# Kernel tuning notes

Measured on AMD Instinct MI355X. Metric: run time of the kernel, lower is better.

Reference implementation:

```python
import jax, jax.numpy as jnp
import numpy as np

N, E, F_IN, HID, HEADS, CLASSES = 50000, 800000, 128, 128, 4, 2
NEG_SLOPE = 0.2


def _gatv2_layer(x, Wl, Wr, att, bias, src, dst, heads, concat):
    # PyG GATv2Conv (share_weights=False, eval mode):
    #   e_ij = att . leaky_relu(Wl x_j + Wr x_i); alpha = segment_softmax over dst;
    #   out_i = sum_j alpha_ij * (Wl x_j)
    n = x.shape[0]
    c = att.shape[-1]
    xl = (x @ Wl).reshape(n, heads, c)   # source transform [N,H,C]
    xr = (x @ Wr).reshape(n, heads, c)   # target transform [N,H,C]
    e = jax.nn.leaky_relu(xl[src] + xr[dst], NEG_SLOPE)      # [E,H,C]
    logits = jnp.einsum('ehc,hc->eh', e, att)                # [E,H]
    m = jax.ops.segment_max(logits, dst, num_segments=n)     # stable softmax per dst
    p = jnp.exp(logits - m[dst])
    denom = jax.ops.segment_sum(p, dst, num_segments=n)
    alpha = p / (denom[dst] + 1e-16)                         # [E,H]
    out = jax.ops.segment_sum(alpha[:, :, None] * xl[src], dst, num_segments=n)  # [N,H,C]
    out = out.reshape(n, heads * c) if concat else out.mean(axis=1)
    return out + bias


def setup_inputs() -> dict:
    key = jax.random.key(0)
    ks = jax.random.split(key, 16)
    s = lambda fan_in: 1.0 / np.sqrt(fan_in)
    inp = {
        'x': jax.random.normal(ks[0], (N, F_IN), jnp.float32),
        'edge_idx': jax.random.randint(ks[1], (2, E), 0, N, jnp.int64),
        'w_in': jax.random.normal(ks[2], (F_IN, HID), jnp.float32) * s(F_IN),
        'b_in': jnp.zeros((HID,), jnp.float32),
        'wl1': jax.random.normal(ks[3], (HID, HEADS * HID), jnp.float32) * s(HID),
        'wr1': jax.random.normal(ks[4], (HID, HEADS * HID), jnp.float32) * s(HID),
        'att1': jax.random.normal(ks[5], (HEADS, HID), jnp.float32) * s(HID),
        'b1': jnp.zeros((HEADS * HID,), jnp.float32),
        'wl2': jax.random.normal(ks[6], (HEADS * HID, HID), jnp.float32) * s(HEADS * HID),
        'wr2': jax.random.normal(ks[7], (HEADS * HID, HID), jnp.float32) * s(HEADS * HID),
        'att2': jax.random.normal(ks[8], (1, HID), jnp.float32) * s(HID),
        'b2': jnp.zeros((HID,), jnp.float32),
        'w_out': jax.random.normal(ks[9], (HID, CLASSES), jnp.float32) * s(HID),
        'b_out': jnp.zeros((CLASSES,), jnp.float32),
    }
    return inp


def reference(x, edge_idx, w_in, b_in, wl1, wr1, att1, b1, wl2, wr2, att2, b2, w_out, b_out):
    n = x.shape[0]
    loops = jnp.arange(n, dtype=edge_idx.dtype)  # PyG add_self_loops=True
    src = jnp.concatenate([edge_idx[0], loops])
    dst = jnp.concatenate([edge_idx[1], loops])
    h = jax.nn.elu(x @ w_in + b_in)              # dropout is identity in eval
    h = jax.nn.elu(_gatv2_layer(h, wl1, wr1, att1, b1, src, dst, HEADS, True))
    h = jax.nn.elu(_gatv2_layer(h, wl2, wr2, att2, b2, src, dst, 1, False))
    logits = h @ w_out + b_out
    return jax.nn.log_softmax(logits, axis=1)
```

## Files before the change

kernel.cpp:

```cpp
#include <hip/hip_runtime.h>
#include <hip/hip_bf16.h>
#include <math.h>

#define F_IN   128
#define HID    128
#define HEADS  4
#define HC1    (HEADS*HID)
#define CLASSES 2
#define NEG_SLOPE 0.2f

#define SCAN_CHUNK 2048

typedef __attribute__((ext_vector_type(8))) short short8;
typedef __attribute__((ext_vector_type(4))) float f32x4;

__global__ void zero_int_kernel(int* __restrict__ p, int n) {
    int i = blockIdx.x * blockDim.x + threadIdx.x;
    int stride = gridDim.x * blockDim.x;
    for (; i < n; i += stride) p[i] = 0;
}

__global__ void deg_kernel(const int* __restrict__ dst_arr, int* __restrict__ deg,
                           int E, int N) {
    int e = blockIdx.x * blockDim.x + threadIdx.x;
    if (e >= E) return;
    int d = dst_arr[e];
    if ((unsigned)d >= (unsigned)N) d = 0;
    atomicAdd(&deg[d], 1);
}

__global__ void scan_partial_kernel(const int* __restrict__ deg, int* __restrict__ bsum, int n) {
    __shared__ int sdata[256];
    int b = blockIdx.x, t = threadIdx.x;
    int base = b * SCAN_CHUNK;
    int s = 0;
    for (int i = t; i < SCAN_CHUNK; i += 256) {
        int idx = base + i;
        s += (idx < n) ? deg[idx] : 0;
    }
    sdata[t] = s;
    __syncthreads();
    for (int off = 128; off; off >>= 1) {
        if (t < off) sdata[t] += sdata[t + off];
        __syncthreads();
    }
    if (t == 0) bsum[b] = sdata[0];
}

__global__ void scan_bsums_kernel(int* __restrict__ bsum, int nb, int* __restrict__ row, int n) {
    if (blockIdx.x == 0 && threadIdx.x == 0) {
        int acc = 0;
        for (int i = 0; i < nb; ++i) { int v = bsum[i]; bsum[i] = acc; acc += v; }
        row[n] = acc;
    }
}

__global__ void scan_final_kernel(const int* __restrict__ deg, const int* __restrict__ bsum,
                                  int* __restrict__ row, int* __restrict__ cursor, int n) {
    __shared__ int tsum[256];
    int b = blockIdx.x, t = threadIdx.x;
    int base = b * SCAN_CHUNK + t * 8;
    int local[8];
    int s = 0;
    #pragma unroll
    for (int k = 0; k < 8; ++k) {
        int idx = base + k;
        int v = (idx < n) ? deg[idx] : 0;
        local[k] = s;
        s += v;
    }
    tsum[t] = s;
    __syncthreads();
    for (int off = 1; off < 256; off <<= 1) {
        int v = 0;
        if (t >= off) v = tsum[t - off];
        __syncthreads();
        if (t >= off) tsum[t] += v;
        __syncthreads();
    }
    int texcl = (t == 0) ? 0 : tsum[t - 1];
    int boff = bsum[b];
    #pragma unroll
    for (int k = 0; k < 8; ++k) {
        int idx = base + k;
        if (idx < n) {
            int v = boff + texcl + local[k];
            row[idx] = v;
            cursor[idx] = v;
        }
    }
}

__global__ void scatter_kernel(const int* __restrict__ src_arr, const int* __restrict__ dst_arr,
                               int* __restrict__ cursor, int* __restrict__ src_sorted,
                               int E, int N) {
    int e = blockIdx.x * blockDim.x + threadIdx.x;
    if (e >= E) return;
    int s = src_arr[e], d = dst_arr[e];
    if ((unsigned)s >= (unsigned)N) s = 0;
    if ((unsigned)d >= (unsigned)N) d = 0;
    int pos = atomicAdd(&cursor[d], 1);
    src_sorted[pos] = s;
}

__global__ void transpose_to_bf16_kernel(const float* __restrict__ w,
                                         __hip_bfloat16* __restrict__ wT,
                                         int K, int N) {
    int t = blockIdx.x * blockDim.x + threadIdx.x;
    if (t >= K * N) return;
    int n = t / K, k = t % K;
    wT[t] = __float2bfloat16(w[(size_t)k * N + n]);
}

__global__ void f32_to_bf16_kernel(const float* __restrict__ in,
                                   __hip_bfloat16* __restrict__ outb, int n) {
    int i = blockIdx.x * blockDim.x + threadIdx.x;
    int stride = gridDim.x * blockDim.x;
    short* ob = (short*)outb;
    for (int base = i * 4; base < n; base += stride * 4) {
        float4 v = *(const float4*)(in + base);
        __hip_bfloat16 h0 = __float2bfloat16(v.x);
        __hip_bfloat16 h1 = __float2bfloat16(v.y);
        __hip_bfloat16 h2 = __float2bfloat16(v.z);
        __hip_bfloat16 h3 = __float2bfloat16(v.w);
        short4 sv;
        sv.x = *reinterpret_cast<short*>(&h0);
        sv.y = *reinterpret_cast<short*>(&h1);
        sv.z = *reinterpret_cast<short*>(&h2);
        sv.w = *reinterpret_cast<short*>(&h3);
        *(short4*)(ob + base) = sv;
    }
}

template<int ACT, typename OutT>
__global__ __launch_bounds__(256) void mfma_gemm_kernel(
    const __hip_bfloat16* __restrict__ A,
    const __hip_bfloat16* __restrict__ BT,
    const float* __restrict__ bias,
    OutT* __restrict__ C,
    int M, int K, int N)
{
    constexpr int BM = 128, BN = 64, BK = 64, LDA = 72;
    __shared__ __align__(16) short As[BM * LDA];
    __shared__ __align__(16) short Bs[BN * LDA];

    const int tid  = threadIdx.x;
    const int lane = tid & 63;
    const int wid  = tid >> 6;
    const int wm   = wid >> 1;
    const int wn   = wid & 1;
    const int fr   = lane & 15;
    const int fk   = (lane >> 4) * 8;

    const int row0 = blockIdx.y * BM;
    const int col0 = blockIdx.x * BN;

    const short* Ag = (const short*)A;
    const short* Bg = (const short*)BT;

    f32x4 acc[4][2] = {};

    for (int k0 = 0; k0 < K; k0 += BK) {
        #pragma unroll
        for (int it = 0; it < 4; ++it) {
            int chunk = it * 256 + tid;
            int r = chunk >> 3, c = chunk & 7;
            int gr = row0 + r;
            short8 v = {0, 0, 0, 0, 0, 0, 0, 0};
            if (gr < M) v = *(const short8*)(Ag + (size_t)gr * K + k0 + c * 8);
            *(short8*)(&As[r * LDA + c * 8]) = v;
        }
        #pragma unroll
        for (int it = 0; it < 2; ++it) {
            int chunk = it * 256 + tid;
            int n = chunk >> 3, c = chunk & 7;
            short8 v = *(const short8*)(Bg + (size_t)(col0 + n) * K + k0 + c * 8);
            *(short8*)(&Bs[n * LDA + c * 8]) = v;
        }
        __syncthreads();
        #pragma unroll
        for (int kk = 0; kk < 2; ++kk) {
            short8 af[4], bf[2];
            #pragma unroll
            for (int i = 0; i < 4; ++i)
                af[i] = *(const short8*)(&As[(wm * 64 + i * 16 + fr) * LDA + kk * 32 + fk]);
            #pragma unroll
            for (int j = 0; j < 2; ++j)
                bf[j] = *(const short8*)(&Bs[(wn * 32 + j * 16 + fr) * LDA + kk * 32 + fk]);
            #pragma unroll
            for (int i = 0; i < 4; ++i)
                #pragma unroll
                for (int j = 0; j < 2; ++j)
                    acc[i][j] = __builtin_amdgcn_mfma_f32_16x16x32_bf16(af[i], bf[j], acc[i][j], 0, 0, 0);
        }
        __syncthreads();
    }

    const int crow = row0 + wm * 64;
    const int ccol = col0 + wn * 32;
    #pragma unroll
    for (int i = 0; i < 4; ++i) {
        #pragma unroll
        for (int j = 0; j < 2; ++j) {
            int col = ccol + j * 16 + (lane & 15);
            float bv = bias ? bias[col] : 0.0f;
            #pragma unroll
            for (int reg = 0; reg < 4; ++reg) {
                int r = crow + i * 16 + (lane >> 4) * 4 + reg;
                if (r < M) {
                    float v = acc[i][j][reg] + bv;
                    if (ACT == 1) v = (v > 0.0f) ? v : expm1f(v);
                    C[(size_t)r * N + col] = (OutT)v;
                }
            }
        }
    }
}

__global__ __launch_bounds__(256) void gatv2_l1_fused_kernel(
    const __hip_bfloat16* __restrict__ xlr,
    const int* __restrict__ row, const int* __restrict__ src_sorted,
    const float* __restrict__ att, const float* __restrict__ b1,
    __hip_bfloat16* __restrict__ out1, int N)
{
    int d = blockIdx.x * 4 + (threadIdx.x >> 6);
    if (d >= N) return;
    int lane = threadIdx.x & 63;
    int cbase = lane * 8;
    const short* base = (const short*)xlr;

    float xrd[8], attv[8];
    {
        uint4 raw = *reinterpret_cast<const uint4*>(base + (size_t)d * 1024 + 512 + cbase);
        const unsigned* u = reinterpret_cast<const unsigned*>(&raw);
        #pragma unroll
        for (int j = 0; j < 4; ++j) {
            xrd[2 * j]     = __uint_as_float(u[j] << 16);
            xrd[2 * j + 1] = __uint_as_float(u[j] & 0xffff0000u);
        }
        #pragma unroll
        for (int k = 0; k < 8; ++k) attv[k] = att[cbase + k];
    }

    float m = -__builtin_huge_valf();
    float s = 0.0f;
    float o[8] = {};

    int rs = row[d], re = row[d + 1];

    uint4 raw = *reinterpret_cast<const uint4*>(base + (size_t)d * 1024 + cbase);
    for (int it = rs - 1; it < re; ++it) {
        uint4 cur = raw;
        if (it + 1 < re) {
            int sn = src_sorted[it + 1];
            raw = *reinterpret_cast<const uint4*>(base + (size_t)sn * 1024 + cbase);
        }
        float v[8];
        const unsigned* u = reinterpret_cast<const unsigned*>(&cur);
        #pragma unroll
        for (int j = 0; j < 4; ++j) {
            v[2 * j]     = __uint_as_float(u[j] << 16);
            v[2 * j + 1] = __uint_as_float(u[j] & 0xffff0000u);
        }
        float t = 0.0f;
        #pragma unroll
        for (int k = 0; k < 8; ++k) {
            float e = v[k] + xrd[k];
            e = (e > 0.0f) ? e : NEG_SLOPE * e;
            t = fmaf(e, attv[k], t);
        }
        t += __shfl_xor(t, 1);
        t += __shfl_xor(t, 2);
        t += __shfl_xor(t, 4);
        t += __shfl_xor(t, 8);
        if (t > m) {
            float r = __expf(m - t);
            s *= r;
            #pragma unroll
            for (int k = 0; k < 8; ++k) o[k] *= r;
            m = t;
        }
        float p = __expf(t - m);
        s += p;
        #pragma unroll
        for (int k = 0; k < 8; ++k) o[k] = fmaf(p, v[k], o[k]);
    }

    float inv = 1.0f / (s + 1e-16f);
    short8 sv;
    #pragma unroll
    for (int k = 0; k < 8; ++k) {
        float val = o[k] * inv + b1[cbase + k];
        val = (val > 0.0f) ? val : expm1f(val);
        __hip_bfloat16 hb = __float2bfloat16(val);
        sv[k] = *reinterpret_cast<short*>(&hb);
    }
    *(short8*)((short*)out1 + (size_t)d * HC1 + cbase) = sv;
}

__global__ __launch_bounds__(256) void gatv2_l2_final_kernel(
    const __hip_bfloat16* __restrict__ xlr2,
    const int* __restrict__ row, const int* __restrict__ src_sorted,
    const float* __restrict__ att2, const float* __restrict__ b2,
    const float* __restrict__ w_out, const float* __restrict__ b_out,
    float* __restrict__ out, int N)
{
    int d = blockIdx.x * 4 + (threadIdx.x >> 6);
    if (d >= N) return;
    int lane = threadIdx.x & 63;
    int c0 = lane * 2;
    const short* base = (const short*)xlr2;

    unsigned xr_raw = *reinterpret_cast<const unsigned*>(base + (size_t)d * 256 + 128 + c0);
    float xrd0 = __uint_as_float(xr_raw << 16);
    float xrd1 = __uint_as_float(xr_raw & 0xffff0000u);
    float2 attv = *reinterpret_cast<const float2*>(att2 + c0);

    float m = -__builtin_huge_valf();
    float s = 0.0f;
    float o0 = 0.0f, o1 = 0.0f;

    int rs = row[d], re = row[d + 1];
    unsigned raw = *reinterpret_cast<const unsigned*>(base + (size_t)d * 256 + c0);
    for (int it = rs - 1; it < re; ++it) {
        unsigned cur = raw;
        if (it + 1 < re) {
            int sn = src_sorted[it + 1];
            raw = *reinterpret_cast<const unsigned*>(base + (size_t)sn * 256 + c0);
        }
        float v0 = __uint_as_float(cur << 16);
        float v1 = __uint_as_float(cur & 0xffff0000u);
        float e0 = v0 + xrd0; e0 = (e0 > 0.0f) ? e0 : NEG_SLOPE * e0;
        float e1 = v1 + xrd1; e1 = (e1 > 0.0f) ? e1 : NEG_SLOPE * e1;
        float t = fmaf(e0, attv.x, e1 * attv.y);
        #pragma unroll
        for (int off = 32; off; off >>= 1) t += __shfl_xor(t, off);
        if (t > m) {
            float r = __expf(m - t);
            s *= r; o0 *= r; o1 *= r;
            m = t;
        }
        float p = __expf(t - m);
        s += p;
        o0 = fmaf(p, v0, o0);
        o1 = fmaf(p, v1, o1);
    }

    float inv = 1.0f / (s + 1e-16f);
    float h0v = o0 * inv + b2[c0];
    float h1v = o1 * inv + b2[c0 + 1];
    h0v = (h0v > 0.0f) ? h0v : expm1f(h0v);
    h1v = (h1v > 0.0f) ? h1v : expm1f(h1v);

    float a0 = fmaf(h0v, w_out[c0 * 2 + 0], h1v * w_out[(c0 + 1) * 2 + 0]);
    float a1 = fmaf(h0v, w_out[c0 * 2 + 1], h1v * w_out[(c0 + 1) * 2 + 1]);
    #pragma unroll
    for (int off = 32; off; off >>= 1) {
        a0 += __shfl_xor(a0, off);
        a1 += __shfl_xor(a1, off);
    }
    if (lane == 0) {
        float z0 = a0 + b_out[0];
        float z1 = a1 + b_out[1];
        float mx = fmaxf(z0, z1);
        float lse = mx + logf(__expf(z0 - mx) + __expf(z1 - mx));
        out[(size_t)d * CLASSES + 0] = z0 - lse;
        out[(size_t)d * CLASSES + 1] = z1 - lse;
    }
}

extern "C" void kernel_launch(void* const* d_in, const int* in_sizes, int n_in,
                              void* d_out, int out_size, void* d_ws, size_t ws_size,
                              hipStream_t stream)
{
    const float* x     = (const float*)d_in[0];
    const int*   eidx  = (const int*)d_in[1];
    const float* w_in  = (const float*)d_in[2];
    const float* b_in  = (const float*)d_in[3];
    const float* wl1   = (const float*)d_in[4];
    const float* wr1   = (const float*)d_in[5];
    const float* att1  = (const float*)d_in[6];
    const float* b1    = (const float*)d_in[7];
    const float* wl2   = (const float*)d_in[8];
    const float* wr2   = (const float*)d_in[9];
    const float* att2  = (const float*)d_in[10];
    const float* b2    = (const float*)d_in[11];
    const float* w_out = (const float*)d_in[12];
    const float* b_out = (const float*)d_in[13];
    float* out = (float*)d_out;

    const int N = in_sizes[0] / F_IN;
    const int E = in_sizes[1] / 2;
    const int* src_arr = eidx;
    const int* dst_arr = eidx + E;

    size_t off = 0;
    auto alloc = [&](size_t bytes) -> char* {
        char* ptr = (char*)d_ws + off;
        off += (bytes + 255) & ~(size_t)255;
        return ptr;
    };
    int* row        = (int*)alloc((size_t)(N + 1) * 4);
    int* cursor     = (int*)alloc((size_t)N * 4);
    int* deg        = (int*)alloc((size_t)N * 4);
    int* bsum       = (int*)alloc(64 * 4);
    int* src_sorted = (int*)alloc((size_t)E * 4);
    __hip_bfloat16* w_inT = (__hip_bfloat16*)alloc((size_t)F_IN * HID * 2);
    __hip_bfloat16* wT1   = (__hip_bfloat16*)alloc((size_t)2 * HC1 * HID * 2);
    __hip_bfloat16* wT2   = (__hip_bfloat16*)alloc((size_t)2 * HID * HC1 * 2);
    __hip_bfloat16* xb    = (__hip_bfloat16*)alloc((size_t)N * F_IN * 2);
    __hip_bfloat16* h0b   = (__hip_bfloat16*)alloc((size_t)N * HID * 2);
    __hip_bfloat16* xlr1  = (__hip_bfloat16*)alloc((size_t)N * 2 * HC1 * 2);
    __hip_bfloat16* out1  = (__hip_bfloat16*)alloc((size_t)N * HC1 * 2);

    __hip_bfloat16* xlr2 = xlr1;

    dim3 blk(256);
    const int NB_SCAN = (N + SCAN_CHUNK - 1) / SCAN_CHUNK;

    hipLaunchKernelGGL(zero_int_kernel, dim3(64), blk, 0, stream, deg, N);
    hipLaunchKernelGGL(deg_kernel, dim3((E + 255) / 256), blk, 0, stream, dst_arr, deg, E, N);
    hipLaunchKernelGGL(scan_partial_kernel, dim3(NB_SCAN), blk, 0, stream, deg, bsum, N);
    hipLaunchKernelGGL(scan_bsums_kernel, dim3(1), blk, 0, stream, bsum, NB_SCAN, row, N);
    hipLaunchKernelGGL(scan_final_kernel, dim3(NB_SCAN), blk, 0, stream, deg, bsum, row, cursor, N);
    hipLaunchKernelGGL(scatter_kernel, dim3((E + 255) / 256), blk, 0, stream,
                       src_arr, dst_arr, cursor, src_sorted, E, N);

    {
        dim3 gw((HID * HC1 + 255) / 256);
        dim3 gwi((F_IN * HID + 255) / 256);
        hipLaunchKernelGGL(transpose_to_bf16_kernel, gwi, blk, 0, stream, w_in, w_inT, F_IN, HID);
        hipLaunchKernelGGL(transpose_to_bf16_kernel, gw, blk, 0, stream, wl1, wT1, HID, HC1);
        hipLaunchKernelGGL(transpose_to_bf16_kernel, gw, blk, 0, stream, wr1, wT1 + (size_t)HC1 * HID, HID, HC1);
        hipLaunchKernelGGL(transpose_to_bf16_kernel, gw, blk, 0, stream, wl2, wT2, HC1, HID);
        hipLaunchKernelGGL(transpose_to_bf16_kernel, gw, blk, 0, stream, wr2, wT2 + (size_t)HID * HC1, HC1, HID);
    }

    hipLaunchKernelGGL(f32_to_bf16_kernel, dim3(2048), blk, 0, stream, x, xb, N * F_IN);
    {
        dim3 grid(HID / 64, (N + 127) / 128);
        hipLaunchKernelGGL((mfma_gemm_kernel<1, __hip_bfloat16>), grid, blk, 0, stream,
                           xb, w_inT, b_in, h0b, N, F_IN, HID);
    }
    {
        dim3 grid(2 * HC1 / 64, (N + 127) / 128);
        hipLaunchKernelGGL((mfma_gemm_kernel<0, __hip_bfloat16>), grid, blk, 0, stream,
                           h0b, wT1, (const float*)nullptr, xlr1, N, HID, 2 * HC1);
    }
    {
        dim3 grid((N + 3) / 4);
        hipLaunchKernelGGL(gatv2_l1_fused_kernel, grid, blk, 0, stream,
                           xlr1, row, src_sorted, att1, b1, out1, N);
    }
    {
        dim3 grid(2 * HID / 64, (N + 127) / 128);
        hipLaunchKernelGGL((mfma_gemm_kernel<0, __hip_bfloat16>), grid, blk, 0, stream,
                           out1, wT2, (const float*)nullptr, xlr2, N, HC1, 2 * HID);
    }
    {
        dim3 grid((N + 3) / 4);
        hipLaunchKernelGGL(gatv2_l2_final_kernel, grid, blk, 0, stream,
                           xlr2, row, src_sorted, att2, b2, w_out, b_out, out, N);
    }
}
```

Before: 603.2 us.

## Split xl/xr buffers, widen GEMM tile, merge weight prep, use exp2 softmax

Splits the interleaved xl/xr projection buffer into separate contiguous arrays so the gather kernels read rows with a smaller stride (HC1 or HID instead of 1024 or 256). Source rows then pack more densely for cache reuse. The GEMM tile grows from 128x64 to 128x128, reusing each A tile across more columns at the cost of more accumulator registers. The five weight-transpose launches merge into one kernel, and layer-2 outputs reuse the xb and h0b buffers. The softmax folds log2(e) into the attention vector so it can use exp2f, and leaky_relu becomes fmaxf.

```diff
diff --git a/kernel.cpp b/kernel.cpp
--- a/kernel.cpp
+++ b/kernel.cpp
@@ -8,6 +8,7 @@
 #define HC1    (HEADS*HID)
 #define CLASSES 2
 #define NEG_SLOPE 0.2f
+#define LOG2E 1.44269504088896340736f
 
 #define SCAN_CHUNK 2048
 
@@ -103,13 +104,25 @@
     src_sorted[pos] = s;
 }
 
-__global__ void transpose_to_bf16_kernel(const float* __restrict__ w,
-                                         __hip_bfloat16* __restrict__ wT,
-                                         int K, int N) {
+__global__ void weights_prep_kernel(
+    const float* __restrict__ w_in, const float* __restrict__ wl1,
+    const float* __restrict__ wr1, const float* __restrict__ wl2,
+    const float* __restrict__ wr2,
+    __hip_bfloat16* __restrict__ w_inT, __hip_bfloat16* __restrict__ wT1l,
+    __hip_bfloat16* __restrict__ wT1r, __hip_bfloat16* __restrict__ wT2l,
+    __hip_bfloat16* __restrict__ wT2r)
+{
     int t = blockIdx.x * blockDim.x + threadIdx.x;
-    if (t >= K * N) return;
-    int n = t / K, k = t % K;
-    wT[t] = __float2bfloat16(w[(size_t)k * N + n]);
+    const int S0 = 128 * 128, S1 = 128 * 512;
+    const float* w; __hip_bfloat16* wT; int K, Nn, idx;
+    if (t < S0)                { w = w_in; wT = w_inT; K = 128; Nn = 128; idx = t; }
+    else if (t < S0 + S1)      { w = wl1;  wT = wT1l;  K = 128; Nn = 512; idx = t - S0; }
+    else if (t < S0 + 2 * S1)  { w = wr1;  wT = wT1r;  K = 128; Nn = 512; idx = t - S0 - S1; }
+    else if (t < S0 + 3 * S1)  { w = wl2;  wT = wT2l;  K = 512; Nn = 128; idx = t - S0 - 2 * S1; }
+    else if (t < S0 + 4 * S1)  { w = wr2;  wT = wT2r;  K = 512; Nn = 128; idx = t - S0 - 3 * S1; }
+    else return;
+    int n = idx / K, k = idx % K;
+    wT[idx] = __float2bfloat16(w[(size_t)k * Nn + n]);
 }
 
 __global__ void f32_to_bf16_kernel(const float* __restrict__ in,
@@ -140,7 +153,7 @@
     OutT* __restrict__ C,
     int M, int K, int N)
 {
-    constexpr int BM = 128, BN = 64, BK = 64, LDA = 72;
+    constexpr int BM = 128, BN = 128, BK = 64, LDA = 72;
     __shared__ __align__(16) short As[BM * LDA];
     __shared__ __align__(16) short Bs[BN * LDA];
 
@@ -158,7 +171,7 @@
     const short* Ag = (const short*)A;
     const short* Bg = (const short*)BT;
 
-    f32x4 acc[4][2] = {};
+    f32x4 acc[4][4] = {};
 
     for (int k0 = 0; k0 < K; k0 += BK) {
         #pragma unroll
@@ -171,7 +184,7 @@
             *(short8*)(&As[r * LDA + c * 8]) = v;
         }
         #pragma unroll
-        for (int it = 0; it < 2; ++it) {
+        for (int it = 0; it < 4; ++it) {
             int chunk = it * 256 + tid;
             int n = chunk >> 3, c = chunk & 7;
             short8 v = *(const short8*)(Bg + (size_t)(col0 + n) * K + k0 + c * 8);
@@ -180,28 +193,28 @@
         __syncthreads();
         #pragma unroll
         for (int kk = 0; kk < 2; ++kk) {
-            short8 af[4], bf[2];
+            short8 af[4], bf[4];
             #pragma unroll
             for (int i = 0; i < 4; ++i)
                 af[i] = *(const short8*)(&As[(wm * 64 + i * 16 + fr) * LDA + kk * 32 + fk]);
             #pragma unroll
-            for (int j = 0; j < 2; ++j)
-                bf[j] = *(const short8*)(&Bs[(wn * 32 + j * 16 + fr) * LDA + kk * 32 + fk]);
+            for (int j = 0; j < 4; ++j)
+                bf[j] = *(const short8*)(&Bs[(wn * 64 + j * 16 + fr) * LDA + kk * 32 + fk]);
             #pragma unroll
             for (int i = 0; i < 4; ++i)
                 #pragma unroll
-                for (int j = 0; j < 2; ++j)
+                for (int j = 0; j < 4; ++j)
                     acc[i][j] = __builtin_amdgcn_mfma_f32_16x16x32_bf16(af[i], bf[j], acc[i][j], 0, 0, 0);
         }
         __syncthreads();
     }
 
     const int crow = row0 + wm * 64;
-    const int ccol = col0 + wn * 32;
+    const int ccol = col0 + wn * 64;
     #pragma unroll
     for (int i = 0; i < 4; ++i) {
         #pragma unroll
-        for (int j = 0; j < 2; ++j) {
+        for (int j = 0; j < 4; ++j) {
             int col = ccol + j * 16 + (lane & 15);
             float bv = bias ? bias[col] : 0.0f;
             #pragma unroll
@@ -218,7 +231,7 @@
 }
 
 __global__ __launch_bounds__(256) void gatv2_l1_fused_kernel(
-    const __hip_bfloat16* __restrict__ xlr,
+    const __hip_bfloat16* __restrict__ xl, const __hip_bfloat16* __restrict__ xr,
     const int* __restrict__ row, const int* __restrict__ src_sorted,
     const float* __restrict__ att, const float* __restrict__ b1,
     __hip_bfloat16* __restrict__ out1, int N)
@@ -227,11 +240,11 @@
     if (d >= N) return;
     int lane = threadIdx.x & 63;
     int cbase = lane * 8;
-    const short* base = (const short*)xlr;
+    const short* xlb = (const short*)xl;
 
     float xrd[8], attv[8];
     {
-        uint4 raw = *reinterpret_cast<const uint4*>(base + (size_t)d * 1024 + 512 + cbase);
+        uint4 raw = *reinterpret_cast<const uint4*>((const short*)xr + (size_t)d * HC1 + cbase);
         const unsigned* u = reinterpret_cast<const unsigned*>(&raw);
         #pragma unroll
         for (int j = 0; j < 4; ++j) {
@@ -239,7 +252,7 @@
             xrd[2 * j + 1] = __uint_as_float(u[j] & 0xffff0000u);
         }
         #pragma unroll
-        for (int k = 0; k < 8; ++k) attv[k] = att[cbase + k];
+        for (int k = 0; k < 8; ++k) attv[k] = att[cbase + k] * LOG2E;
     }
 
     float m = -__builtin_huge_valf();
@@ -248,12 +261,12 @@
 
     int rs = row[d], re = row[d + 1];
 
-    uint4 raw = *reinterpret_cast<const uint4*>(base + (size_t)d * 1024 + cbase);
+    uint4 raw = *reinterpret_cast<const uint4*>(xlb + (size_t)d * HC1 + cbase);
     for (int it = rs - 1; it < re; ++it) {
         uint4 cur = raw;
         if (it + 1 < re) {
             int sn = src_sorted[it + 1];
-            raw = *reinterpret_cast<const uint4*>(base + (size_t)sn * 1024 + cbase);
+            raw = *reinterpret_cast<const uint4*>(xlb + (size_t)sn * HC1 + cbase);
         }
         float v[8];
         const unsigned* u = reinterpret_cast<const unsigned*>(&cur);
@@ -265,8 +278,8 @@
         float t = 0.0f;
         #pragma unroll
         for (int k = 0; k < 8; ++k) {
-            float e = v[k] + xrd[k];
-            e = (e > 0.0f) ? e : NEG_SLOPE * e;
+            float ek = v[k] + xrd[k];
+            float e = fmaxf(ek, NEG_SLOPE * ek);
             t = fmaf(e, attv[k], t);
         }
         t += __shfl_xor(t, 1);
@@ -274,13 +287,13 @@
         t += __shfl_xor(t, 4);
         t += __shfl_xor(t, 8);
         if (t > m) {
-            float r = __expf(m - t);
+            float r = exp2f(m - t);
             s *= r;
             #pragma unroll
             for (int k = 0; k < 8; ++k) o[k] *= r;
             m = t;
         }
-        float p = __expf(t - m);
+        float p = exp2f(t - m);
         s += p;
         #pragma unroll
         for (int k = 0; k < 8; ++k) o[k] = fmaf(p, v[k], o[k]);
@@ -299,7 +312,7 @@
 }
 
 __global__ __launch_bounds__(256) void gatv2_l2_final_kernel(
-    const __hip_bfloat16* __restrict__ xlr2,
+    const __hip_bfloat16* __restrict__ xl2, const __hip_bfloat16* __restrict__ xr2,
     const int* __restrict__ row, const int* __restrict__ src_sorted,
     const float* __restrict__ att2, const float* __restrict__ b2,
     const float* __restrict__ w_out, const float* __restrict__ b_out,
@@ -309,38 +322,39 @@
     if (d >= N) return;
     int lane = threadIdx.x & 63;
     int c0 = lane * 2;
-    const short* base = (const short*)xlr2;
-
-    unsigned xr_raw = *reinterpret_cast<const unsigned*>(base + (size_t)d * 256 + 128 + c0);
+    const short* xlb = (const short*)xl2;
+
+    unsigned xr_raw = *reinterpret_cast<const unsigned*>((const short*)xr2 + (size_t)d * HID + c0);
     float xrd0 = __uint_as_float(xr_raw << 16);
     float xrd1 = __uint_as_float(xr_raw & 0xffff0000u);
-    float2 attv = *reinterpret_cast<const float2*>(att2 + c0);
+    float a2x = att2[c0] * LOG2E;
+    float a2y = att2[c0 + 1] * LOG2E;
 
     float m = -__builtin_huge_valf();
     float s = 0.0f;
     float o0 = 0.0f, o1 = 0.0f;
 
     int rs = row[d], re = row[d + 1];
-    unsigned raw = *reinterpret_cast<const unsigned*>(base + (size_t)d * 256 + c0);
+    unsigned raw = *reinterpret_cast<const unsigned*>(xlb + (size_t)d * HID + c0);
     for (int it = rs - 1; it < re; ++it) {
         unsigned cur = raw;
         if (it + 1 < re) {
             int sn = src_sorted[it + 1];
-            raw = *reinterpret_cast<const unsigned*>(base + (size_t)sn * 256 + c0);
+            raw = *reinterpret_cast<const unsigned*>(xlb + (size_t)sn * HID + c0);
         }
         float v0 = __uint_as_float(cur << 16);
         float v1 = __uint_as_float(cur & 0xffff0000u);
-        float e0 = v0 + xrd0; e0 = (e0 > 0.0f) ? e0 : NEG_SLOPE * e0;
-        float e1 = v1 + xrd1; e1 = (e1 > 0.0f) ? e1 : NEG_SLOPE * e1;
-        float t = fmaf(e0, attv.x, e1 * attv.y);
+        float e0 = v0 + xrd0; e0 = fmaxf(e0, NEG_SLOPE * e0);
+        float e1 = v1 + xrd1; e1 = fmaxf(e1, NEG_SLOPE * e1);
+        float t = fmaf(e0, a2x, e1 * a2y);
         #pragma unroll
         for (int off = 32; off; off >>= 1) t += __shfl_xor(t, off);
         if (t > m) {
-            float r = __expf(m - t);
+            float r = exp2f(m - t);
             s *= r; o0 *= r; o1 *= r;
             m = t;
         }
-        float p = __expf(t - m);
+        float p = exp2f(t - m);
         s += p;
         o0 = fmaf(p, v0, o0);
         o1 = fmaf(p, v1, o1);
@@ -406,14 +420,18 @@
     int* bsum       = (int*)alloc(64 * 4);
     int* src_sorted = (int*)alloc((size_t)E * 4);
     __hip_bfloat16* w_inT = (__hip_bfloat16*)alloc((size_t)F_IN * HID * 2);
-    __hip_bfloat16* wT1   = (__hip_bfloat16*)alloc((size_t)2 * HC1 * HID * 2);
-    __hip_bfloat16* wT2   = (__hip_bfloat16*)alloc((size_t)2 * HID * HC1 * 2);
+    __hip_bfloat16* wT1l  = (__hip_bfloat16*)alloc((size_t)HID * HC1 * 2);
+    __hip_bfloat16* wT1r  = (__hip_bfloat16*)alloc((size_t)HID * HC1 * 2);
+    __hip_bfloat16* wT2l  = (__hip_bfloat16*)alloc((size_t)HC1 * HID * 2);
+    __hip_bfloat16* wT2r  = (__hip_bfloat16*)alloc((size_t)HC1 * HID * 2);
     __hip_bfloat16* xb    = (__hip_bfloat16*)alloc((size_t)N * F_IN * 2);
     __hip_bfloat16* h0b   = (__hip_bfloat16*)alloc((size_t)N * HID * 2);
-    __hip_bfloat16* xlr1  = (__hip_bfloat16*)alloc((size_t)N * 2 * HC1 * 2);
+    __hip_bfloat16* xl1   = (__hip_bfloat16*)alloc((size_t)N * HC1 * 2);
+    __hip_bfloat16* xr1   = (__hip_bfloat16*)alloc((size_t)N * HC1 * 2);
     __hip_bfloat16* out1  = (__hip_bfloat16*)alloc((size_t)N * HC1 * 2);
 
-    __hip_bfloat16* xlr2 = xlr1;
+    __hip_bfloat16* xl2 = xb;
+    __hip_bfloat16* xr2 = h0b;
 
     dim3 blk(256);
     const int NB_SCAN = (N + SCAN_CHUNK - 1) / SCAN_CHUNK;
@@ -427,39 +445,38 @@
                        src_arr, dst_arr, cursor, src_sorted, E, N);
 
     {
-        dim3 gw((HID * HC1 + 255) / 256);
-        dim3 gwi((F_IN * HID + 255) / 256);
-        hipLaunchKernelGGL(transpose_to_bf16_kernel, gwi, blk, 0, stream, w_in, w_inT, F_IN, HID);
-        hipLaunchKernelGGL(transpose_to_bf16_kernel, gw, blk, 0, stream, wl1, wT1, HID, HC1);
-        hipLaunchKernelGGL(transpose_to_bf16_kernel, gw, blk, 0, stream, wr1, wT1 + (size_t)HC1 * HID, HID, HC1);
-        hipLaunchKernelGGL(transpose_to_bf16_kernel, gw, blk, 0, stream, wl2, wT2, HC1, HID);
-        hipLaunchKernelGGL(transpose_to_bf16_kernel, gw, blk, 0, stream, wr2, wT2 + (size_t)HID * HC1, HC1, HID);
-    }
-
-    hipLaunchKernelGGL(f32_to_bf16_kernel, dim3(2048), blk, 0, stream, x, xb, N * F_IN);
-    {
-        dim3 grid(HID / 64, (N + 127) / 128);
+        int total = 128 * 128 + 4 * 128 * 512;
+        hipLaunchKernelGGL(weights_prep_kernel, dim3((total + 255) / 256), blk, 0, stream,
+                           w_in, wl1, wr1, wl2, wr2, w_inT, wT1l, wT1r, wT2l, wT2r);
+        hipLaunchKernelGGL(f32_to_bf16_kernel, dim3(2048), blk, 0, stream, x, xb, N * F_IN);
+    }
+    {
+        dim3 grid(HID / 128, (N + 127) / 128);
         hipLaunchKernelGGL((mfma_gemm_kernel<1, __hip_bfloat16>), grid, blk, 0, stream,
                            xb, w_inT, b_in, h0b, N, F_IN, HID);
     }
     {
-        dim3 grid(2 * HC1 / 64, (N + 127) / 128);
+        dim3 grid(HC1 / 128, (N + 127) / 128);
         hipLaunchKernelGGL((mfma_gemm_kernel<0, __hip_bfloat16>), grid, blk, 0, stream,
-                           h0b, wT1, (const float*)nullptr, xlr1, N, HID, 2 * HC1);
+                           h0b, wT1l, (const float*)nullptr, xl1, N, HID, HC1);
+        hipLaunchKernelGGL((mfma_gemm_kernel<0, __hip_bfloat16>), grid, blk, 0, stream,
+                           h0b, wT1r, (const float*)nullptr, xr1, N, HID, HC1);
     }
     {
         dim3 grid((N + 3) / 4);
         hipLaunchKernelGGL(gatv2_l1_fused_kernel, grid, blk, 0, stream,
-                           xlr1, row, src_sorted, att1, b1, out1, N);
-    }
-    {
-        dim3 grid(2 * HID / 64, (N + 127) / 128);
+                           xl1, xr1, row, src_sorted, att1, b1, out1, N);
+    }
+    {
+        dim3 grid(HID / 128, (N + 127) / 128);
         hipLaunchKernelGGL((mfma_gemm_kernel<0, __hip_bfloat16>), grid, blk, 0, stream,
-                           out1, wT2, (const float*)nullptr, xlr2, N, HC1, 2 * HID);
+                           out1, wT2l, (const float*)nullptr, xl2, N, HC1, HID);
+        hipLaunchKernelGGL((mfma_gemm_kernel<0, __hip_bfloat16>), grid, blk, 0, stream,
+                           out1, wT2r, (const float*)nullptr, xr2, N, HC1, HID);
     }
     {
         dim3 grid((N + 3) / 4);
         hipLaunchKernelGGL(gatv2_l2_final_kernel, grid, blk, 0, stream,
-                           xlr2, row, src_sorted, att2, b2, w_out, b_out, out, N);
-    }
-}
+                           xl2, xr2, row, src_sorted, att2, b2, w_out, b_out, out, N);
+    }
+}
```

After: 588.4 us. 2.5% less time.
